# Kernel tuning notes

Hardware: AMD Instinct MI355X
Metric: run time of the kernel (lower is better)

The kernel has to match this reference:

```python
import jax, jax.numpy as jnp
import numpy as np

N = 8192      # nodes
E = 131072    # global edges
SDIM = 256    # scalar channels
VDIM = 64     # vector channels
EDIM = 128    # edge feature dim
L = 5         # num_layers
DIN = 2 * SDIM + EDIM + 4        # [s_src, s_tgt, e, d, a, |p_src|, |p_tgt|]
DOUT = SDIM + 2 * VDIM + 1 + EDIM  # [m_s, w_v1, w_v2, w_p, e_new]
HID = SDIM


def setup_inputs() -> dict:
    key = jax.random.key(0)
    ks = jax.random.split(key, 12)
    s = jax.random.normal(ks[0], (N, SDIM), jnp.float32)
    v = 0.1 * jax.random.normal(ks[1], (N, 3, VDIM), jnp.float32)
    p = 3.0 * jax.random.normal(ks[2], (N, 3), jnp.float32)
    e = jax.random.normal(ks[3], (E, EDIM), jnp.float32)
    edge_index = jax.random.randint(ks[4], (2, E), 0, N, dtype=jnp.int32)
    W1 = jax.random.normal(ks[5], (L, DIN, HID), jnp.float32) / np.sqrt(DIN)
    W2 = jax.random.normal(ks[6], (L, HID, DOUT), jnp.float32) / np.sqrt(HID)
    U1 = jax.random.normal(ks[7], (L, SDIM, SDIM), jnp.float32) / np.sqrt(SDIM)
    U2 = jax.random.normal(ks[8], (L, SDIM, SDIM), jnp.float32) / np.sqrt(SDIM)
    return {
        's': s, 'v': v, 'p': p, 'e': e, 'edge_index': edge_index,
        'ln_g': jnp.ones((L, SDIM), jnp.float32),
        'ln_b': jnp.zeros((L, SDIM), jnp.float32),
        'W1': W1, 'b1': jnp.zeros((L, HID), jnp.float32),
        'W2': W2, 'b2': jnp.zeros((L, DOUT), jnp.float32),
        'U1': U1, 'bU1': jnp.zeros((L, SDIM), jnp.float32),
        'U2': U2, 'bU2': jnp.zeros((L, SDIM), jnp.float32),
    }


def _edge_attrs(edge_index, pos):
    # Faithful to calculate_edge_attrs (sqrt=True, no ligand-pocket branch)
    src, tgt = edge_index[0], edge_index[1]
    r = pos[tgt] - pos[src]                                   # [E,3]
    a = jnp.sum(pos[tgt] * pos[src], axis=-1)                 # [E]
    d = jnp.sqrt(jnp.clip(jnp.sum(r * r, axis=-1), 1e-6, None))
    r_norm = r / (1.0 + d[:, None])
    return d, a, r_norm


def reference(s, v, p, e, edge_index, ln_g, ln_b, W1, b1, W2, b2, U1, bU1, U2, bU2):
    src, tgt = edge_index[0], edge_index[1]
    d, a, rn = _edge_attrs(edge_index, p)
    # in-degree counts for 'mean' vector/position aggregation
    cnt = jnp.clip(jax.ops.segment_sum(jnp.ones((E,), s.dtype), tgt, num_segments=N), 1.0)
    for i in range(L):
        # LayerNorm on scalar channels (vectors passed through)
        mu = jnp.mean(s, axis=-1, keepdims=True)
        var = jnp.mean((s - mu) ** 2, axis=-1, keepdims=True)
        s_ln = ln_g[i] * (s - mu) * jax.lax.rsqrt(var + 1e-5) + ln_b[i]
        pn = jnp.linalg.norm(p, axis=-1, keepdims=True)       # use_pos_norm features
        # gather-compute edge messages
        feat = jnp.concatenate(
            [s_ln[src], s_ln[tgt], e, d[:, None], a[:, None], pn[src], pn[tgt]], axis=-1)
        h = jax.nn.silu(feat @ W1[i] + b1[i])                 # [E,HID]
        out = h @ W2[i] + b2[i]                               # [E,DOUT]
        m_s = out[:, :SDIM]
        wv1 = out[:, SDIM:SDIM + VDIM]
        wv2 = out[:, SDIM + VDIM:SDIM + 2 * VDIM]
        wp = out[:, SDIM + 2 * VDIM:SDIM + 2 * VDIM + 1]
        e_new = out[:, SDIM + 2 * VDIM + 1:]
        has_v = 0.0 if i == 0 else 1.0                        # has_v_in = (i > 0)
        m_v = has_v * wv1[:, None, :] * v[src] + wv2[:, None, :] * rn[:, :, None]  # [E,3,VDIM]
        m_p = jnp.tanh(wp) * rn                               # [E,3]
        # scatter-aggregate (sum for scalars, mean for vectors/positions)
        s = s + jax.ops.segment_sum(m_s, tgt, num_segments=N)
        v = v + jax.ops.segment_sum(m_v, tgt, num_segments=N) / cnt[:, None, None]
        p = p + jax.ops.segment_sum(m_p, tgt, num_segments=N) / cnt[:, None]
        if i < L - 1:                                         # use_mlp_update = (i < num_layers - 1)
            s = s + jax.nn.silu(s @ U1[i] + bU1[i]) @ U2[i] + bU2[i]
        e = jax.nn.silu(e_new)
        # recompute_edge_attributes=True: redo gather/distance math on new positions
        d, a, rn = _edge_attrs(edge_index, p)
    return s, v, e, p
```

## Files before the change

### kernel.cpp

```cpp
#include <hip/hip_runtime.h>
#include <hip/hip_bf16.h>

namespace {

constexpr int NN   = 8192;
constexpr int NE   = 131072;
constexpr int SD   = 256;
constexpr int ED   = 128;
constexpr int NL   = 5;
constexpr int DINc = 644;
constexpr int KE   = 160;
constexpr int TE   = 5;
constexpr int T2   = 8;
constexpr int DOUTc= 513;
constexpr int HIDc = 256;

typedef __bf16 bf16x8 __attribute__((ext_vector_type(8)));
typedef float  f32x4  __attribute__((ext_vector_type(4)));

__device__ __forceinline__ float siluf(float x) { return x / (1.0f + __expf(-x)); }

__device__ __forceinline__ void gl_lds16(const void* gsrc, void* lds_uniform_base) {
  __builtin_amdgcn_global_load_lds(
      (const __attribute__((address_space(1))) unsigned int*)gsrc,
      (__attribute__((address_space(3))) unsigned int*)lds_uniform_base, 16, 0, 0);
}

__device__ __forceinline__ void wait_vm4() {
  asm volatile("s_waitcnt vmcnt(4)" ::: "memory");
  __builtin_amdgcn_sched_barrier(0);
}
__device__ __forceinline__ void wait_vm0() {
  asm volatile("s_waitcnt vmcnt(0)" ::: "memory");
  __builtin_amdgcn_sched_barrier(0);
}

__device__ __host__ __forceinline__ int swz(int kc) { return (kc * 5) & 7; }
__device__ __forceinline__ int apos(int kc, int row) { return kc * 64  + (row ^ swz(kc)); }
__device__ __forceinline__ int bpos(int kc, int n)   { return kc * 256 + (n   ^ swz(kc)); }

enum { SRC_BF16 = 1 };

struct GemmArgs {
  const __hip_bfloat16* Wt;
  const float* bias;
  const __hip_bfloat16* Abf;
  __hip_bfloat16* bf_out;
  const __hip_bfloat16* Wtb;
  const float* biasb;
  __hip_bfloat16* bf_outb;
  int dual;
};

__device__ __forceinline__ uint4 cvt8f(const float* p) {
  alignas(16) __hip_bfloat16 t8[8];
#pragma unroll
  for (int i = 0; i < 8; i++) t8[i] = __float2bfloat16(p[i]);
  return *(const uint4*)t8;
}

template<int KTOT, int BM>
__global__ __launch_bounds__(256) void gemm_k(GemmArgs g) {
  constexpr int T = KTOT / 32;
  constexpr int NC = KTOT / 8;
  constexpr int RPT = 256 / BM;
  constexpr int RMASK = RPT - 1;
  __shared__ alignas(16) unsigned short Apan[NC * BM * 8];
  __shared__ alignas(16) unsigned short Bsh[2][4 * 256 * 8];
  const int tid = threadIdx.x, lane = tid & 63, wave = tid >> 6;
  const int l16 = lane & 15, lhi = lane >> 4;
  const __hip_bfloat16* wtp = g.Wt;
  const float* biasp = g.bias;
  __hip_bfloat16* outp = g.bf_out;
  int blk = blockIdx.x;
  {
    const int half = gridDim.x >> 1;
    if (g.dual && blk >= half) { blk -= half; wtp = g.Wtb; biasp = g.biasb; outp = g.bf_outb; }
  }
  const int row0 = blk * BM;
  const int ar = tid / RPT, aq = tid % RPT;
  const int arow = row0 + ar;
  f32x4 acc[BM / 16][4] = {};

  auto issueB = [&](int t, int buf) {
    const __hip_bfloat16* src = wtp + (size_t)t * 1024 * 8;
    unsigned short* dst = &Bsh[buf][0];
#pragma unroll
    for (int i = 0; i < 4; i++)
      gl_lds16(src + (size_t)(i * 256 + wave * 64 + lane) * 8, dst + (i * 256 + wave * 64) * 8);
  };

  issueB(0, 0);
#pragma unroll
  for (int j = 0; j < NC / RPT; j++) {
    const int c = j * RPT + aq;
    uint4 o = *(const uint4*)(g.Abf + (size_t)arow * KTOT + c * 8);
    *(uint4*)&Apan[(c * BM + (ar ^ swz(aq))) * 8] = o;
  }
  __syncthreads();

  int cur = 0;
  for (int t = 0; t < T; ++t) {
    if (t + 1 < T) { issueB(t + 1, cur ^ 1); wait_vm4(); }
    else           { wait_vm0(); }
    bf16x8 bfr[4];
#pragma unroll
    for (int f = 0; f < 4; f++)
      bfr[f] = *(const bf16x8*)&Bsh[cur][bpos(lhi, wave * 64 + f * 16 + l16) * 8];
#pragma unroll
    for (int fr = 0; fr < BM / 16; fr++) {
      const int kc = t * 4 + lhi;
      const bf16x8 afr = *(const bf16x8*)&Apan[(kc * BM + ((fr * 16 + l16) ^ swz(kc & RMASK))) * 8];
#pragma unroll
      for (int fc = 0; fc < 4; fc++)
        acc[fr][fc] = __builtin_amdgcn_mfma_f32_16x16x32_bf16(afr, bfr[fc], acc[fr][fc], 0, 0, 0);
    }
    cur ^= 1;
  }

#pragma unroll
  for (int fr = 0; fr < BM / 16; fr++) {
#pragma unroll
    for (int fc = 0; fc < 4; fc++) {
      const int n = wave * 64 + fc * 16 + l16;
#pragma unroll
      for (int r = 0; r < 4; r++) {
        const int row = row0 + fr * 16 + lhi * 4 + r;
        outp[(size_t)row * HIDc + n] = __float2bfloat16(acc[fr][fc][r] + biasp[n]);
      }
    }
  }
}

struct Node3Args {
  const __hip_bfloat16* W2a;
  const __hip_bfloat16* U1s;
  const __hip_bfloat16* U2s;
  const __hip_bfloat16* W1an;
  const __hip_bfloat16* W1bn;
  const float* b2L;
  const float* bU1;
  const float* bU2;
  const float* b1n;
  const float* lng;
  const float* lnb;
  const float* Hagg;
  const int* rawcnt;
  float* s_out;
  __hip_bfloat16* p1;
  __hip_bfloat16* p2;
};

template<int LAST>
__global__ __launch_bounds__(256) void node3_k(Node3Args g) {
  constexpr int BM = 32, RPT = 8, NC = 32, T = 8;
  __shared__ alignas(16) unsigned short Apan[NC * BM * 8];
  __shared__ alignas(16) unsigned short Bsh[2][4 * 256 * 8];
  __shared__ float red[2][4][32];
  const int tid = threadIdx.x, lane = tid & 63, wave = tid >> 6;
  const int l16 = lane & 15, lhi = lane >> 4;
  const int row0 = blockIdx.x * BM;
  const int ar = tid >> 3, aq = tid & 7;

  auto issueB = [&](const __hip_bfloat16* W, int t, int buf) {
    const __hip_bfloat16* src = W + (size_t)t * 1024 * 8;
    unsigned short* dst = &Bsh[buf][0];
#pragma unroll
    for (int i = 0; i < 4; i++)
      gl_lds16(src + (size_t)(i * 256 + wave * 64 + lane) * 8, dst + (i * 256 + wave * 64) * 8);
  };

  f32x4 acc[4][2];
  auto kloop = [&](const __hip_bfloat16* W) {
#pragma unroll
    for (int i = 0; i < 4; i++)
#pragma unroll
      for (int j = 0; j < 2; j++) acc[i][j] = f32x4{0.f, 0.f, 0.f, 0.f};
    int cur = 0;
    for (int t = 0; t < T; ++t) {
      if (t + 1 < T) { issueB(W, t + 1, cur ^ 1); wait_vm4(); }
      else           { wait_vm0(); }
      bf16x8 wfr[4], afr[2];
#pragma unroll
      for (int f = 0; f < 4; f++)
        wfr[f] = *(const bf16x8*)&Bsh[cur][bpos(lhi, wave * 64 + f * 16 + l16) * 8];
#pragma unroll
      for (int f = 0; f < 2; f++) {
        const int kc = t * 4 + lhi;
        afr[f] = *(const bf16x8*)&Apan[(kc * BM + ((f * 16 + l16) ^ swz(kc & 7))) * 8];
      }
#pragma unroll
      for (int fr = 0; fr < 4; fr++)
#pragma unroll
        for (int fc = 0; fc < 2; fc++)
          acc[fr][fc] = __builtin_amdgcn_mfma_f32_16x16x32_bf16(wfr[fr], afr[fc], acc[fr][fc], 0, 0, 0);
      cur ^= 1;
    }
  };

  issueB(g.W2a, 0, 0);
#pragma unroll
  for (int j = 0; j < NC / RPT; j++) {
    const int c = j * RPT + aq;
    uint4 o = cvt8f(g.Hagg + (size_t)(row0 + ar) * SD + c * 8);
    *(uint4*)&Apan[(c * BM + (ar ^ swz(aq))) * 8] = o;
  }
  __syncthreads();

  kloop(g.W2a);
  __syncthreads();
  if constexpr (!LAST) issueB(g.U1s, 0, 0);

#pragma unroll
  for (int fr = 0; fr < 4; fr++) {
    const int nb = wave * 64 + fr * 16 + lhi * 4;
    const int kc = nb >> 3, off = nb & 7;
    const f32x4 b4 = *(const f32x4*)(g.b2L + nb);
#pragma unroll
    for (int fc = 0; fc < 2; fc++) {
      const int row = fc * 16 + l16;
      const float rc = (float)g.rawcnt[row0 + row];
      float* sp = g.s_out + (size_t)(row0 + row) * SD + nb;
      f32x4 sold = *(const f32x4*)sp;
      alignas(8) __hip_bfloat16 hb[4];
      f32x4 s1;
#pragma unroll
      for (int r = 0; r < 4; r++) {
        s1[r] = sold[r] + acc[fr][fc][r] + rc * b4[r];
        hb[r] = __float2bfloat16(s1[r]);
      }
      *(f32x4*)sp = s1;
      if constexpr (!LAST)
        *(uint2*)&Apan[(kc * BM + (row ^ swz(kc & 7))) * 8 + off] = *(const uint2*)hb;
    }
  }
  if constexpr (LAST) return;

  __syncthreads();

  kloop(g.U1s);
  __syncthreads();
  issueB(g.U2s, 0, 0);
#pragma unroll
  for (int fr = 0; fr < 4; fr++) {
    const int nb = wave * 64 + fr * 16 + lhi * 4;
    const int kc = nb >> 3, off = nb & 7;
    const f32x4 b4 = *(const f32x4*)(g.bU1 + nb);
#pragma unroll
    for (int fc = 0; fc < 2; fc++) {
      const int row = fc * 16 + l16;
      alignas(8) __hip_bfloat16 hb[4];
#pragma unroll
      for (int r = 0; r < 4; r++)
        hb[r] = __float2bfloat16(siluf(acc[fr][fc][r] + b4[r]));
      *(uint2*)&Apan[(kc * BM + (row ^ swz(kc & 7))) * 8 + off] = *(const uint2*)hb;
    }
  }
  __syncthreads();

  kloop(g.U2s);
  float psum[2] = {0.f, 0.f}, psq[2] = {0.f, 0.f};
#pragma unroll
  for (int fr = 0; fr < 4; fr++) {
    const int nb = wave * 64 + fr * 16 + lhi * 4;
    const f32x4 b4 = *(const f32x4*)(g.bU2 + nb);
#pragma unroll
    for (int fc = 0; fc < 2; fc++) {
      const int row = fc * 16 + l16;
      float* sp = g.s_out + (size_t)(row0 + row) * SD + nb;
      f32x4 sv = *(const f32x4*)sp;
#pragma unroll
      for (int r = 0; r < 4; r++) {
        sv[r] += acc[fr][fc][r] + b4[r];
        psum[fc] += sv[r];
        psq[fc] += sv[r] * sv[r];
      }
      *(f32x4*)sp = sv;
      acc[fr][fc] = sv;
    }
  }
#pragma unroll
  for (int fc = 0; fc < 2; fc++) {
    psum[fc] += __shfl_xor(psum[fc], 16); psum[fc] += __shfl_xor(psum[fc], 32);
    psq[fc]  += __shfl_xor(psq[fc], 16);  psq[fc]  += __shfl_xor(psq[fc], 32);
  }
  if (lane < 16) {
    red[0][wave][lane] = psum[0]; red[0][wave][16 + lane] = psum[1];
    red[1][wave][lane] = psq[0];  red[1][wave][16 + lane] = psq[1];
  }
  __syncthreads();

  float mu2[2], rs2[2];
#pragma unroll
  for (int fc = 0; fc < 2; fc++) {
    const int ri = fc * 16 + l16;
    const float S = red[0][0][ri] + red[0][1][ri] + red[0][2][ri] + red[0][3][ri];
    const float Q = red[1][0][ri] + red[1][1][ri] + red[1][2][ri] + red[1][3][ri];
    const float mu = S * (1.0f / SD);
    const float var = Q * (1.0f / SD) - mu * mu;
    mu2[fc] = mu; rs2[fc] = rsqrtf(var + 1e-5f);
  }
#pragma unroll
  for (int fr = 0; fr < 4; fr++) {
    const int nb = wave * 64 + fr * 16 + lhi * 4;
    const int kc = nb >> 3, off = nb & 7;
    const f32x4 g4 = *(const f32x4*)(g.lng + nb);
    const f32x4 bb4 = *(const f32x4*)(g.lnb + nb);
#pragma unroll
    for (int fc = 0; fc < 2; fc++) {
      const int row = fc * 16 + l16;
      alignas(8) __hip_bfloat16 hb[4];
#pragma unroll
      for (int r = 0; r < 4; r++)
        hb[r] = __float2bfloat16(g4[r] * (acc[fr][fc][r] - mu2[fc]) * rs2[fc] + bb4[r]);
      *(uint2*)&Apan[(kc * BM + (row ^ swz(kc & 7))) * 8 + off] = *(const uint2*)hb;
    }
  }
  issueB(g.W1an, 0, 0);
  __syncthreads();

  kloop(g.W1an);
#pragma unroll
  for (int fr = 0; fr < 4; fr++) {
    const int nb = wave * 64 + fr * 16 + lhi * 4;
    const f32x4 b4 = *(const f32x4*)(g.b1n + nb);
#pragma unroll
    for (int fc = 0; fc < 2; fc++) {
      const int row = fc * 16 + l16;
      alignas(8) __hip_bfloat16 hb[4];
#pragma unroll
      for (int r = 0; r < 4; r++)
        hb[r] = __float2bfloat16(acc[fr][fc][r] + b4[r]);
      *(uint2*)(g.p1 + (size_t)(row0 + row) * SD + nb) = *(const uint2*)hb;
    }
  }
  issueB(g.W1bn, 0, 0);
  kloop(g.W1bn);
#pragma unroll
  for (int fr = 0; fr < 4; fr++) {
    const int nb = wave * 64 + fr * 16 + lhi * 4;
#pragma unroll
    for (int fc = 0; fc < 2; fc++) {
      const int row = fc * 16 + l16;
      alignas(8) __hip_bfloat16 hb[4];
#pragma unroll
      for (int r = 0; r < 4; r++)
        hb[r] = __float2bfloat16(acc[fr][fc][r]);
      *(uint2*)(g.p2 + (size_t)(row0 + row) * SD + nb) = *(const uint2*)hb;
    }
  }
}

struct FusedArgs {
  const __hip_bfloat16* W1e;
  const __hip_bfloat16* W2s;
  const float* b2L;
  const int* src; const int* tgt;
  const int* rank;
  const float* pos;
  const __hip_bfloat16* e_bf;
  const __hip_bfloat16* p1;
  const __hip_bfloat16* p2;
  const __hip_bfloat16* w384;
  float* rnp;
  float* mp;
  __hip_bfloat16* h_out;
  __hip_bfloat16* wv_out;
  __hip_bfloat16* e_bf_out;
  float* e_f32_out;
  int write_e_f32;
};

__global__ __launch_bounds__(256) void fused_k(FusedArgs g) {
  __shared__ alignas(16) unsigned short Ash[4 * 64 * 8];
  __shared__ alignas(16) unsigned short Bsh[2][4 * 256 * 8];
  __shared__ alignas(16) unsigned short Hsh[32 * 64 * 8];
  __shared__ float wps[4][64];
  __shared__ float RnL[64][3];
  __shared__ unsigned int EdL[64][2];
  __shared__ int Rk[64];
  const int tid = threadIdx.x, lane = tid & 63, wave = tid >> 6;
  const int l16 = lane & 15, lhi = lane >> 4;
  const int row0 = blockIdx.x * 64;
  const int ar = tid >> 2, aq = tid & 3;
  const int arow = row0 + ar;
  const int sn = g.src[arow], tn = g.tgt[arow];

  auto issueW = [&](const __hip_bfloat16* W, int t, int buf) {
    const __hip_bfloat16* src = W + (size_t)t * 1024 * 8;
    unsigned short* dst = &Bsh[buf][0];
#pragma unroll
    for (int i = 0; i < 4; i++)
      gl_lds16(src + (size_t)(i * 256 + wave * 64 + lane) * 8, dst + (i * 256 + wave * 64) * 8);
  };
  auto loadA = [&](int t, uint4& o) {
    if (t < 4) {
      o = *(const uint4*)(g.e_bf + (size_t)arow * ED + t * 32 + aq * 8);
    } else {
      o.x = o.y = o.z = o.w = 0;
      if (aq == 0) { o.x = EdL[ar][0]; o.y = EdL[ar][1]; }
    }
  };

  uint4 a;
  loadA(0, a);
  issueW(g.W1e, 0, 0);

  if (tid < 64) {
    const int e = row0 + tid;
    const int rk = g.rank[e];
    Rk[tid] = rk;
    const int s_ = g.src[e], t_ = g.tgt[e];
    const float sx = g.pos[s_ * 3], sy = g.pos[s_ * 3 + 1], sz = g.pos[s_ * 3 + 2];
    const float tx = g.pos[t_ * 3], ty = g.pos[t_ * 3 + 1], tz = g.pos[t_ * 3 + 2];
    const float rx = tx - sx, ry = ty - sy, rz = tz - sz;
    const float av = tx * sx + ty * sy + tz * sz;
    const float rr = rx * rx + ry * ry + rz * rz;
    const float d = sqrtf(fmaxf(rr, 1e-6f));
    const float inv = 1.0f / (1.0f + d);
    const float r0 = rx * inv, r1 = ry * inv, r2 = rz * inv;
    RnL[tid][0] = r0; RnL[tid][1] = r1; RnL[tid][2] = r2;
    g.rnp[rk * 3] = r0; g.rnp[rk * 3 + 1] = r1; g.rnp[rk * 3 + 2] = r2;
    alignas(8) __hip_bfloat16 q[4];
    q[0] = __float2bfloat16(d);
    q[1] = __float2bfloat16(av);
    q[2] = __float2bfloat16(sqrtf(sx * sx + sy * sy + sz * sz));
    q[3] = __float2bfloat16(sqrtf(tx * tx + ty * ty + tz * tz));
    EdL[tid][0] = ((const unsigned*)q)[0];
    EdL[tid][1] = ((const unsigned*)q)[1];
  }

#pragma unroll
  for (int j = 0; j < 8; j++) {
    const int c = j * 4 + aq;
    uint4 r1 = *(const uint4*)(g.p1 + (size_t)sn * SD + c * 8);
    uint4 r2 = *(const uint4*)(g.p2 + (size_t)tn * SD + c * 8);
    const __hip_bfloat16* h1 = (const __hip_bfloat16*)&r1;
    const __hip_bfloat16* h2 = (const __hip_bfloat16*)&r2;
    alignas(16) __hip_bfloat16 o8[8];
#pragma unroll
    for (int m = 0; m < 8; m++)
      o8[m] = __float2bfloat16(__bfloat162float(h1[m]) + __bfloat162float(h2[m]));
    *(uint4*)&Hsh[(c * 64 + (ar ^ swz(aq))) * 8] = *(const uint4*)o8;
  }

  f32x4 acc1[4][4] = {};
  int cur = 0;
  for (int t = 0; t < TE; ++t) {
    *(uint4*)&Ash[apos(aq, ar) * 8] = a;
    __syncthreads();
    if (t + 1 < TE) { issueW(g.W1e, t + 1, cur ^ 1); loadA(t + 1, a); }
    bf16x8 wfr[4], efr[4];
#pragma unroll
    for (int f = 0; f < 4; f++) {
      wfr[f] = *(const bf16x8*)&Bsh[cur][bpos(lhi, wave * 64 + f * 16 + l16) * 8];
      efr[f] = *(const bf16x8*)&Ash[apos(lhi, f * 16 + l16) * 8];
    }
#pragma unroll
    for (int fr = 0; fr < 4; fr++)
#pragma unroll
      for (int fc = 0; fc < 4; fc++)
        acc1[fr][fc] = __builtin_amdgcn_mfma_f32_16x16x32_bf16(wfr[fr], efr[fc], acc1[fr][fc], 0, 0, 0);
    __syncthreads();
    cur ^= 1;
  }

  issueW(g.W2s, 0, 0);

  float pw[4] = {0.f, 0.f, 0.f, 0.f};
#pragma unroll
  for (int fr = 0; fr < 4; fr++) {
    const int nb = wave * 64 + fr * 16 + lhi * 4;
    const int kc = nb >> 3, off = nb & 7;
    uint2 wr = *(const uint2*)(g.w384 + nb);
    const __hip_bfloat16* w4 = (const __hip_bfloat16*)&wr;
#pragma unroll
    for (int fc = 0; fc < 4; fc++) {
      const int row = fc * 16 + l16;
      unsigned short* slot = &Hsh[(kc * 64 + (row ^ swz(kc & 3))) * 8 + off];
      uint2 pr = *(const uint2*)slot;
      const __hip_bfloat16* pp = (const __hip_bfloat16*)&pr;
      alignas(8) __hip_bfloat16 hb[4];
#pragma unroll
      for (int r = 0; r < 4; r++) {
        const float hv = siluf(acc1[fr][fc][r] + __bfloat162float(pp[r]));
        hb[r] = __float2bfloat16(hv);
        pw[fc] += hv * __bfloat162float(w4[r]);
      }
      *(uint2*)slot = *(const uint2*)hb;
      *(uint2*)(g.h_out + (size_t)Rk[row] * HIDc + nb) = *(const uint2*)hb;
    }
  }

#pragma unroll
  for (int fc = 0; fc < 4; fc++) {
    pw[fc] += __shfl_xor(pw[fc], 16);
    pw[fc] += __shfl_xor(pw[fc], 32);
  }
  if (lane < 16) {
#pragma unroll
    for (int fc = 0; fc < 4; fc++) wps[wave][fc * 16 + lane] = pw[fc];
  }
  __syncthreads();
  if (tid < 64) {
    const float s = wps[0][tid] + wps[1][tid] + wps[2][tid] + wps[3][tid];
    const float wpt = tanhf(s + g.b2L[384]);
    const int rk = Rk[tid];
#pragma unroll
    for (int c = 0; c < 3; c++)
      g.mp[(size_t)rk * 3 + c] = wpt * RnL[tid][c];
  }

  f32x4 acc2[4][4] = {};
  cur = 0;
  for (int t = 0; t < T2; ++t) {
    if (t + 1 < T2) { issueW(g.W2s, t + 1, cur ^ 1); wait_vm4(); }
    else            { wait_vm0(); }
    bf16x8 afr[4], bfr[4];
#pragma unroll
    for (int f = 0; f < 4; f++) {
      const int kc = t * 4 + lhi;
      afr[f] = *(const bf16x8*)&Hsh[(kc * 64 + ((f * 16 + l16) ^ swz(lhi))) * 8];
      bfr[f] = *(const bf16x8*)&Bsh[cur][bpos(lhi, wave * 64 + f * 16 + l16) * 8];
    }
#pragma unroll
    for (int fr = 0; fr < 4; fr++)
#pragma unroll
      for (int fc = 0; fc < 4; fc++)
        acc2[fr][fc] = __builtin_amdgcn_mfma_f32_16x16x32_bf16(afr[fr], bfr[fc], acc2[fr][fc], 0, 0, 0);
    cur ^= 1;
  }

#pragma unroll
  for (int fr = 0; fr < 4; fr++) {
#pragma unroll
    for (int fc = 0; fc < 4; fc++) {
      const int n = wave * 64 + fc * 16 + l16;
#pragma unroll
      for (int r = 0; r < 4; r++) {
        const int lr = fr * 16 + lhi * 4 + r;
        const int row = row0 + lr;
        const float valf = acc2[fr][fc][r];
        if (n < 128) {
          g.wv_out[(size_t)Rk[lr] * 128 + n] = __float2bfloat16(valf + g.b2L[256 + n]);
        } else {
          const float sv = siluf(valf + g.b2L[257 + n]);
          g.e_bf_out[(size_t)row * ED + (n - 128)] = __float2bfloat16(sv);
          if (g.write_e_f32) g.e_f32_out[(size_t)row * ED + (n - 128)] = sv;
        }
      }
    }
  }
}

__global__ __launch_bounds__(256) void ln_k(const float* __restrict__ s,
                                            const float* __restrict__ gl, const float* __restrict__ bl,
                                            __hip_bfloat16* __restrict__ s_ln) {
  const int wave = threadIdx.x >> 6, lane = threadIdx.x & 63;
  const int node = blockIdx.x * 4 + wave;
  const float* srow = s + (size_t)node * SD;
  float x[4], sum = 0.f, sq = 0.f;
#pragma unroll
  for (int i = 0; i < 4; i++) { x[i] = srow[lane * 4 + i]; sum += x[i]; sq += x[i] * x[i]; }
#pragma unroll
  for (int off = 1; off < 64; off <<= 1) { sum += __shfl_xor(sum, off); sq += __shfl_xor(sq, off); }
  const float mu = sum * (1.0f / SD);
  const float var = sq * (1.0f / SD) - mu * mu;
  const float rstd = rsqrtf(var + 1e-5f);
#pragma unroll
  for (int i = 0; i < 4; i++) {
    const int c = lane * 4 + i;
    s_ln[(size_t)node * SD + c] = __float2bfloat16(gl[c] * (x[i] - mu) * rstd + bl[c]);
  }
}

__global__ void cvt_e_k(const float* __restrict__ e, __hip_bfloat16* __restrict__ ebf) {
  const int i = blockIdx.x * blockDim.x + threadIdx.x;
  const float* p = e + (size_t)i * 8;
  alignas(16) __hip_bfloat16 t8[8];
#pragma unroll
  for (int j = 0; j < 8; j++) t8[j] = __float2bfloat16(p[j]);
  *(uint4*)(ebf + (size_t)i * 8) = *(const uint4*)t8;
}

__global__ void count_k(const int* __restrict__ tgt, int* __restrict__ rawcnt) {
  const int e = blockIdx.x * blockDim.x + threadIdx.x;
  if (e < NE) atomicAdd(&rawcnt[tgt[e]], 1);
}

__global__ __launch_bounds__(256) void scan_k(const int* __restrict__ rawcnt, int* __restrict__ off) {
  __shared__ int ts[256];
  const int tid = threadIdx.x;
  const int base = tid * 32;
  int local[32];
  int s = 0;
#pragma unroll
  for (int i = 0; i < 32; i++) { local[i] = s; s += rawcnt[base + i]; }
  ts[tid] = s;
  __syncthreads();
  if (tid == 0) {
    int acc = 0;
    for (int i = 0; i < 256; i++) { int t = ts[i]; ts[i] = acc; acc += t; }
    off[NN] = acc;
  }
  __syncthreads();
  const int pre = ts[tid];
#pragma unroll
  for (int i = 0; i < 32; i++) off[base + i] = pre + local[i];
}

__global__ void scatter_k(const int* __restrict__ tgt, const int* __restrict__ srcp,
                          const int* __restrict__ off,
                          int* __restrict__ cursor, int* __restrict__ rank, int* __restrict__ psrc) {
  const int e = blockIdx.x * blockDim.x + threadIdx.x;
  if (e < NE) {
    const int t = tgt[e];
    const int pos = off[t] + atomicAdd(&cursor[t], 1);
    rank[e] = pos;
    psrc[pos] = srcp[e];
  }
}

__global__ __launch_bounds__(256) void agg_k(const int* __restrict__ off, const int* __restrict__ psrc,
                                             const __hip_bfloat16* __restrict__ h,
                                             const __hip_bfloat16* __restrict__ wv,
                                             const float* __restrict__ mp,
                                             const float* __restrict__ rnp,
                                             const float* __restrict__ v_old,
                                             float* __restrict__ v_new,
                                             float* __restrict__ Hagg,
                                             float* __restrict__ p_o,
                                             int hasv) {
  const int n = blockIdx.x;
  const int c = threadIdx.x;
  const int e0 = off[n], e1 = off[n + 1];
  const int c3 = c >> 6, ln = c & 63;
  float hs = 0.f, vs = 0.f, ps = 0.f;
  int j = e0;
  for (; j + 2 <= e1; j += 2) {
    const float h0 = __bfloat162float(h[(size_t)j * HIDc + c]);
    const float h1 = __bfloat162float(h[(size_t)(j + 1) * HIDc + c]);
    hs += h0 + h1;
    if (c < 192) {
      const int s0 = psrc[j], s1 = psrc[j + 1];
      float m0 = __bfloat162float(wv[(size_t)j * 128 + 64 + ln]) * rnp[j * 3 + c3];
      float m1 = __bfloat162float(wv[(size_t)(j + 1) * 128 + 64 + ln]) * rnp[(j + 1) * 3 + c3];
      if (hasv) {
        m0 += __bfloat162float(wv[(size_t)j * 128 + ln]) * v_old[(size_t)s0 * 192 + c];
        m1 += __bfloat162float(wv[(size_t)(j + 1) * 128 + ln]) * v_old[(size_t)s1 * 192 + c];
      }
      vs += m0 + m1;
    } else if (c < 195) {
      ps += mp[j * 3 + (c - 192)] + mp[(j + 1) * 3 + (c - 192)];
    }
  }
  for (; j < e1; j++) {
    hs += __bfloat162float(h[(size_t)j * HIDc + c]);
    if (c < 192) {
      float mv = __bfloat162float(wv[(size_t)j * 128 + 64 + ln]) * rnp[j * 3 + c3];
      if (hasv) mv += __bfloat162float(wv[(size_t)j * 128 + ln]) * v_old[(size_t)psrc[j] * 192 + c];
      vs += mv;
    } else if (c < 195) {
      ps += mp[j * 3 + (c - 192)];
    }
  }
  Hagg[(size_t)n * HIDc + c] = hs;
  const float inv = 1.0f / fmaxf((float)(e1 - e0), 1.0f);
  if (c < 192)      v_new[(size_t)n * 192 + c] = v_old[(size_t)n * 192 + c] + vs * inv;
  else if (c < 195) p_o[n * 3 + (c - 192)]    += ps * inv;
}

__global__ void zero_k(float* __restrict__ ptr, int n) {
  const int i = blockIdx.x * blockDim.x + threadIdx.x;
  if (i < n) ptr[i] = 0.f;
}

__global__ void prep_w1abs_k(const float* __restrict__ W1, __hip_bfloat16* __restrict__ W1aS,
                             __hip_bfloat16* __restrict__ W1bS) {
  const int idx = blockIdx.x * blockDim.x + threadIdx.x;
  if (idx >= NL * T2 * 1024) return;
  const int p = idx & 1023, t = (idx >> 10) % T2, l = idx / (T2 * 1024);
  const int kc = p >> 8, n = (p & 255) ^ swz(kc);
  alignas(16) __hip_bfloat16 a8[8], b8[8];
#pragma unroll
  for (int j = 0; j < 8; j++) {
    const int k = t * 32 + kc * 8 + j;
    a8[j] = __float2bfloat16(W1[((size_t)l * DINc + k) * HIDc + n]);
    b8[j] = __float2bfloat16(W1[((size_t)l * DINc + 256 + k) * HIDc + n]);
  }
  *(uint4*)(W1aS + (size_t)idx * 8) = *(const uint4*)a8;
  *(uint4*)(W1bS + (size_t)idx * 8) = *(const uint4*)b8;
}

__global__ void prep_w1es_k(const float* __restrict__ W1, __hip_bfloat16* __restrict__ W1eS) {
  const int idx = blockIdx.x * blockDim.x + threadIdx.x;
  if (idx >= NL * TE * 1024) return;
  const int p = idx & 1023, t = (idx >> 10) % TE, l = idx / (TE * 1024);
  const int kc = p >> 8, n = (p & 255) ^ swz(kc);
  alignas(16) __hip_bfloat16 e8[8];
#pragma unroll
  for (int j = 0; j < 8; j++) {
    const int k = t * 32 + kc * 8 + j;
    const int row = (k < 128) ? (512 + k) : ((k < 132) ? (640 + (k - 128)) : -1);
    e8[j] = __float2bfloat16(row >= 0 ? W1[((size_t)l * DINc + row) * HIDc + n] : 0.f);
  }
  *(uint4*)(W1eS + (size_t)idx * 8) = *(const uint4*)e8;
}

__global__ void prep_w2s_k(const float* __restrict__ W2, __hip_bfloat16* __restrict__ W2sS,
                           __hip_bfloat16* __restrict__ W2aS) {
  const int idx = blockIdx.x * blockDim.x + threadIdx.x;
  if (idx >= NL * T2 * 1024) return;
  const int p = idx & 1023, t = (idx >> 10) & 7, l = idx >> 13;
  const int kc = p >> 8, n = (p & 255) ^ swz(kc);
  const float* W2l = W2 + (size_t)l * HIDc * DOUTc;
  const int cs = (n < 128) ? (256 + n) : (257 + n);
  alignas(16) __hip_bfloat16 s8[8], a8[8];
#pragma unroll
  for (int j = 0; j < 8; j++) {
    const int k = t * 32 + kc * 8 + j;
    s8[j] = __float2bfloat16(W2l[(size_t)k * DOUTc + cs]);
    a8[j] = __float2bfloat16(W2l[(size_t)k * DOUTc + n]);
  }
  *(uint4*)(W2sS + (size_t)idx * 8) = *(const uint4*)s8;
  *(uint4*)(W2aS + (size_t)idx * 8) = *(const uint4*)a8;
}

__global__ void prep_uts_k(const float* __restrict__ U1, const float* __restrict__ U2,
                           __hip_bfloat16* __restrict__ U1S, __hip_bfloat16* __restrict__ U2S) {
  const int idx = blockIdx.x * blockDim.x + threadIdx.x;
  if (idx >= NL * T2 * 1024) return;
  const int p = idx & 1023, t = (idx >> 10) & 7, l = idx >> 13;
  const int kc = p >> 8, n = (p & 255) ^ swz(kc);
  alignas(16) __hip_bfloat16 u1[8], u2[8];
#pragma unroll
  for (int j = 0; j < 8; j++) {
    const int k = t * 32 + kc * 8 + j;
    u1[j] = __float2bfloat16(U1[((size_t)l * HIDc + k) * HIDc + n]);
    u2[j] = __float2bfloat16(U2[((size_t)l * HIDc + k) * HIDc + n]);
  }
  *(uint4*)(U1S + (size_t)idx * 8) = *(const uint4*)u1;
  *(uint4*)(U2S + (size_t)idx * 8) = *(const uint4*)u2;
}

__global__ void prep_w384_k(const float* __restrict__ W2, __hip_bfloat16* __restrict__ w384) {
  const int idx = blockIdx.x * blockDim.x + threadIdx.x;
  if (idx >= NL * HIDc) return;
  const int k = idx & 255, l = idx >> 8;
  w384[idx] = __float2bfloat16(W2[((size_t)l * HIDc + k) * DOUTc + 384]);
}

}

extern "C" void kernel_launch(void* const* d_in, const int* in_sizes, int n_in,
                              void* d_out, int out_size, void* d_ws, size_t ws_size,
                              hipStream_t stream) {
  (void)in_sizes; (void)n_in; (void)out_size; (void)ws_size;
  const float* s_in = (const float*)d_in[0];
  const float* v_in = (const float*)d_in[1];
  const float* p_in = (const float*)d_in[2];
  const float* e_in = (const float*)d_in[3];
  const int*   ei   = (const int*)d_in[4];
  const float* ln_g = (const float*)d_in[5];
  const float* ln_b = (const float*)d_in[6];
  const float* W1   = (const float*)d_in[7];
  const float* b1   = (const float*)d_in[8];
  const float* W2   = (const float*)d_in[9];
  const float* b2   = (const float*)d_in[10];
  const float* U1   = (const float*)d_in[11];
  const float* bU1  = (const float*)d_in[12];
  const float* U2   = (const float*)d_in[13];
  const float* bU2  = (const float*)d_in[14];

  float* s_o = (float*)d_out;
  float* v_o = s_o + (size_t)NN * SD;
  float* e_o = v_o + (size_t)NN * 192;
  float* p_o = e_o + (size_t)NE * ED;

  const int* srcp = ei;
  const int* tgtp = ei + NE;

  char* wp = (char*)d_ws;
  auto alloc = [&](size_t bytes) -> char* {
    char* r = wp; wp += (bytes + 255) & ~(size_t)255; return r;
  };
  __hip_bfloat16* s_ln = (__hip_bfloat16*)alloc((size_t)NN * SD * 2);
  __hip_bfloat16* hbuf = (__hip_bfloat16*)alloc((size_t)NE * HIDc * 2);
  __hip_bfloat16* ebf  = (__hip_bfloat16*)alloc((size_t)NE * ED * 2);
  __hip_bfloat16* wvbuf= (__hip_bfloat16*)alloc((size_t)NE * 128 * 2);
  __hip_bfloat16* p1buf= (__hip_bfloat16*)alloc((size_t)NN * SD * 2);
  __hip_bfloat16* p2buf= (__hip_bfloat16*)alloc((size_t)NN * SD * 2);
  float* rnpbuf= (float*)alloc((size_t)NE * 3 * 4);
  float* Hagg  = (float*)alloc((size_t)NN * SD * 4);
  float* vprev = (float*)alloc((size_t)NN * 192 * 4);
  float* mpbuf = (float*)alloc((size_t)NE * 3 * 4);
  float* zerobias = (float*)alloc(256 * 4);
  int*   rawcnt= (int*)alloc((size_t)NN * 4);
  int*   offb  = (int*)alloc((size_t)(NN + 1) * 4);
  int*   cursor= (int*)alloc((size_t)NN * 4);
  int*   rankb = (int*)alloc((size_t)NE * 4);
  int*   psrcb = (int*)alloc((size_t)NE * 4);
  __hip_bfloat16* W1aS = (__hip_bfloat16*)alloc((size_t)NL * T2 * 1024 * 8 * 2);
  __hip_bfloat16* W1bS = (__hip_bfloat16*)alloc((size_t)NL * T2 * 1024 * 8 * 2);
  __hip_bfloat16* W1eS = (__hip_bfloat16*)alloc((size_t)NL * TE * 1024 * 8 * 2);
  __hip_bfloat16* W2sS = (__hip_bfloat16*)alloc((size_t)NL * T2 * 1024 * 8 * 2);
  __hip_bfloat16* W2aS = (__hip_bfloat16*)alloc((size_t)NL * T2 * 1024 * 8 * 2);
  __hip_bfloat16* U1S  = (__hip_bfloat16*)alloc((size_t)NL * T2 * 1024 * 8 * 2);
  __hip_bfloat16* U2S  = (__hip_bfloat16*)alloc((size_t)NL * T2 * 1024 * 8 * 2);
  __hip_bfloat16* w384 = (__hip_bfloat16*)alloc((size_t)NL * HIDc * 2);

  hipMemcpyAsync(s_o, s_in, (size_t)NN * SD * 4, hipMemcpyDeviceToDevice, stream);
  hipMemcpyAsync(vprev, v_in, (size_t)NN * 192 * 4, hipMemcpyDeviceToDevice, stream);
  hipMemcpyAsync(p_o, p_in, (size_t)NN * 3 * 4, hipMemcpyDeviceToDevice, stream);

  prep_w1abs_k<<<(NL * T2 * 1024 + 255) / 256, 256, 0, stream>>>(W1, W1aS, W1bS);
  prep_w1es_k<<<(NL * TE * 1024 + 255) / 256, 256, 0, stream>>>(W1, W1eS);
  prep_w2s_k<<<(NL * T2 * 1024 + 255) / 256, 256, 0, stream>>>(W2, W2sS, W2aS);
  prep_uts_k<<<(NL * T2 * 1024 + 255) / 256, 256, 0, stream>>>(U1, U2, U1S, U2S);
  prep_w384_k<<<(NL * HIDc + 255) / 256, 256, 0, stream>>>(W2, w384);
  cvt_e_k<<<NE * ED / 8 / 256, 256, 0, stream>>>(e_in, ebf);
  zero_k<<<1, 256, 0, stream>>>(zerobias, 256);

  zero_k<<<(NN + 255) / 256, 256, 0, stream>>>((float*)rawcnt, NN);
  zero_k<<<(NN + 255) / 256, 256, 0, stream>>>((float*)cursor, NN);
  count_k<<<NE / 256, 256, 0, stream>>>(tgtp, rawcnt);
  scan_k<<<1, 256, 0, stream>>>(rawcnt, offb);
  scatter_k<<<NE / 256, 256, 0, stream>>>(tgtp, srcp, offb, cursor, rankb, psrcb);

  ln_k<<<NN / 4, 256, 0, stream>>>(s_o, ln_g, ln_b, s_ln);
  GemmArgs gp{};
  gp.Wt = W1aS; gp.bias = b1; gp.bf_out = p1buf;
  gp.Wtb = W1bS; gp.biasb = zerobias; gp.bf_outb = p2buf;
  gp.Abf = s_ln; gp.dual = 1;
  gemm_k<256, 64><<<2 * NN / 64, 256, 0, stream>>>(gp);

  for (int l = 0; l < NL; l++) {
    FusedArgs gf{};
    gf.W1e = W1eS + (size_t)l * TE * 1024 * 8;
    gf.W2s = W2sS + (size_t)l * T2 * 1024 * 8;
    gf.b2L = b2 + l * DOUTc;
    gf.src = srcp; gf.tgt = tgtp; gf.rank = rankb;
    gf.pos = p_o; gf.e_bf = ebf;
    gf.p1 = p1buf; gf.p2 = p2buf; gf.w384 = w384 + l * HIDc;
    gf.rnp = rnpbuf; gf.mp = mpbuf;
    gf.h_out = hbuf; gf.wv_out = wvbuf; gf.e_bf_out = ebf; gf.e_f32_out = e_o;
    gf.write_e_f32 = (l == NL - 1) ? 1 : 0;
    fused_k<<<NE / 64, 256, 0, stream>>>(gf);

    const float* vold = (l & 1) ? (const float*)v_o : (const float*)vprev;
    float* vnew = (l & 1) ? vprev : v_o;
    agg_k<<<NN, 256, 0, stream>>>(offb, psrcb, hbuf, wvbuf, mpbuf, rnpbuf,
                                  vold, vnew, Hagg, p_o, (l > 0) ? 1 : 0);

    Node3Args gn{};
    gn.W2a = W2aS + (size_t)l * T2 * 1024 * 8;
    gn.U1s = U1S + (size_t)l * T2 * 1024 * 8;
    gn.U2s = U2S + (size_t)l * T2 * 1024 * 8;
    gn.b2L = b2 + l * DOUTc; gn.bU1 = bU1 + l * HIDc; gn.bU2 = bU2 + l * HIDc;
    gn.Hagg = Hagg; gn.rawcnt = rawcnt; gn.s_out = s_o;
    if (l < NL - 1) {
      gn.W1an = W1aS + (size_t)(l + 1) * T2 * 1024 * 8;
      gn.W1bn = W1bS + (size_t)(l + 1) * T2 * 1024 * 8;
      gn.b1n = b1 + (l + 1) * HIDc;
      gn.lng = ln_g + (l + 1) * SD; gn.lnb = ln_b + (l + 1) * SD;
      gn.p1 = p1buf; gn.p2 = p2buf;
      node3_k<0><<<NN / 32, 256, 0, stream>>>(gn);
    } else {
      node3_k<1><<<NN / 32, 256, 0, stream>>>(gn);
    }
  }
}
```

Baseline: 1.020 ms.

## Stage whole edge-feature tile in LDS and drop per-step barriers in first GEMM

Loads all edge features and edge attributes into the shared H buffer before the first GEMM. The first GEMM loop then runs without two block barriers per k-step, using vmcnt waits on the async weight loads, like the second GEMM. The gathered node projections are prefetched early into registers and written to LDS after the first GEMM. This removes the separate A buffer and per-step synchronisation, but raises register pressure. Without a barrier, the double-buffered weight tiles may be overwritten while other waves still read them.

```diff
diff --git a/kernel.cpp b/kernel.cpp
--- a/kernel.cpp
+++ b/kernel.cpp
@@ -36,8 +36,8 @@
 }
 
 __device__ __host__ __forceinline__ int swz(int kc) { return (kc * 5) & 7; }
-__device__ __forceinline__ int apos(int kc, int row) { return kc * 64  + (row ^ swz(kc)); }
 __device__ __forceinline__ int bpos(int kc, int n)   { return kc * 256 + (n   ^ swz(kc)); }
+__device__ __forceinline__ int ppos(int kc, int row) { return kc * 64 + (row ^ swz(kc & 3)); }
 
 enum { SRC_BF16 = 1 };
 
@@ -372,12 +372,10 @@
 };
 
 __global__ __launch_bounds__(256) void fused_k(FusedArgs g) {
-  __shared__ alignas(16) unsigned short Ash[4 * 64 * 8];
   __shared__ alignas(16) unsigned short Bsh[2][4 * 256 * 8];
   __shared__ alignas(16) unsigned short Hsh[32 * 64 * 8];
   __shared__ float wps[4][64];
   __shared__ float RnL[64][3];
-  __shared__ unsigned int EdL[64][2];
   __shared__ int Rk[64];
   const int tid = threadIdx.x, lane = tid & 63, wave = tid >> 6;
   const int l16 = lane & 15, lhi = lane >> 4;
@@ -393,18 +391,16 @@
     for (int i = 0; i < 4; i++)
       gl_lds16(src + (size_t)(i * 256 + wave * 64 + lane) * 8, dst + (i * 256 + wave * 64) * 8);
   };
-  auto loadA = [&](int t, uint4& o) {
-    if (t < 4) {
-      o = *(const uint4*)(g.e_bf + (size_t)arow * ED + t * 32 + aq * 8);
-    } else {
-      o.x = o.y = o.z = o.w = 0;
-      if (aq == 0) { o.x = EdL[ar][0]; o.y = EdL[ar][1]; }
-    }
-  };
-
-  uint4 a;
-  loadA(0, a);
+
   issueW(g.W1e, 0, 0);
+
+  uint4 r1[8], r2[8];
+#pragma unroll
+  for (int j = 0; j < 8; j++) {
+    const int c = j * 4 + aq;
+    r1[j] = *(const uint4*)(g.p1 + (size_t)sn * SD + c * 8);
+    r2[j] = *(const uint4*)(g.p2 + (size_t)tn * SD + c * 8);
+  }
 
   if (tid < 64) {
     const int e = row0 + tid;
@@ -418,54 +414,69 @@
     const float rr = rx * rx + ry * ry + rz * rz;
     const float d = sqrtf(fmaxf(rr, 1e-6f));
     const float inv = 1.0f / (1.0f + d);
-    const float r0 = rx * inv, r1 = ry * inv, r2 = rz * inv;
-    RnL[tid][0] = r0; RnL[tid][1] = r1; RnL[tid][2] = r2;
-    g.rnp[rk * 3] = r0; g.rnp[rk * 3 + 1] = r1; g.rnp[rk * 3 + 2] = r2;
-    alignas(8) __hip_bfloat16 q[4];
-    q[0] = __float2bfloat16(d);
-    q[1] = __float2bfloat16(av);
-    q[2] = __float2bfloat16(sqrtf(sx * sx + sy * sy + sz * sz));
-    q[3] = __float2bfloat16(sqrtf(tx * tx + ty * ty + tz * tz));
-    EdL[tid][0] = ((const unsigned*)q)[0];
-    EdL[tid][1] = ((const unsigned*)q)[1];
-  }
-
+    const float r0 = rx * inv, r1v = ry * inv, r2v = rz * inv;
+    RnL[tid][0] = r0; RnL[tid][1] = r1v; RnL[tid][2] = r2v;
+    g.rnp[rk * 3] = r0; g.rnp[rk * 3 + 1] = r1v; g.rnp[rk * 3 + 2] = r2v;
+    alignas(16) __hip_bfloat16 q8[8];
+    q8[0] = __float2bfloat16(d);
+    q8[1] = __float2bfloat16(av);
+    q8[2] = __float2bfloat16(sqrtf(sx * sx + sy * sy + sz * sz));
+    q8[3] = __float2bfloat16(sqrtf(tx * tx + ty * ty + tz * tz));
+    q8[4] = q8[5] = q8[6] = q8[7] = __float2bfloat16(0.0f);
+    *(uint4*)&Hsh[ppos(16, tid) * 8] = *(const uint4*)q8;
+  } else {
+  }
+  if (aq > 0) {
+    uint4 z; z.x = z.y = z.z = z.w = 0;
+    *(uint4*)&Hsh[ppos(16 + aq, ar) * 8] = z;
+  }
+#pragma unroll
+  for (int j = 0; j < 4; j++) {
+    const int c = j * 4 + aq;
+    uint4 o = *(const uint4*)(g.e_bf + (size_t)arow * ED + c * 8);
+    *(uint4*)&Hsh[ppos(c, ar) * 8] = o;
+  }
+  __syncthreads();
+
+  uint4 ps[8];
 #pragma unroll
   for (int j = 0; j < 8; j++) {
-    const int c = j * 4 + aq;
-    uint4 r1 = *(const uint4*)(g.p1 + (size_t)sn * SD + c * 8);
-    uint4 r2 = *(const uint4*)(g.p2 + (size_t)tn * SD + c * 8);
-    const __hip_bfloat16* h1 = (const __hip_bfloat16*)&r1;
-    const __hip_bfloat16* h2 = (const __hip_bfloat16*)&r2;
+    const __hip_bfloat16* h1 = (const __hip_bfloat16*)&r1[j];
+    const __hip_bfloat16* h2 = (const __hip_bfloat16*)&r2[j];
     alignas(16) __hip_bfloat16 o8[8];
 #pragma unroll
     for (int m = 0; m < 8; m++)
       o8[m] = __float2bfloat16(__bfloat162float(h1[m]) + __bfloat162float(h2[m]));
-    *(uint4*)&Hsh[(c * 64 + (ar ^ swz(aq))) * 8] = *(const uint4*)o8;
+    ps[j] = *(const uint4*)o8;
   }
 
   f32x4 acc1[4][4] = {};
   int cur = 0;
   for (int t = 0; t < TE; ++t) {
-    *(uint4*)&Ash[apos(aq, ar) * 8] = a;
-    __syncthreads();
-    if (t + 1 < TE) { issueW(g.W1e, t + 1, cur ^ 1); loadA(t + 1, a); }
+    if (t + 1 < TE) { issueW(g.W1e, t + 1, cur ^ 1); wait_vm4(); }
+    else            { wait_vm0(); }
     bf16x8 wfr[4], efr[4];
 #pragma unroll
     for (int f = 0; f < 4; f++) {
       wfr[f] = *(const bf16x8*)&Bsh[cur][bpos(lhi, wave * 64 + f * 16 + l16) * 8];
-      efr[f] = *(const bf16x8*)&Ash[apos(lhi, f * 16 + l16) * 8];
+      efr[f] = *(const bf16x8*)&Hsh[ppos(t * 4 + lhi, f * 16 + l16) * 8];
     }
 #pragma unroll
     for (int fr = 0; fr < 4; fr++)
 #pragma unroll
       for (int fc = 0; fc < 4; fc++)
         acc1[fr][fc] = __builtin_amdgcn_mfma_f32_16x16x32_bf16(wfr[fr], efr[fc], acc1[fr][fc], 0, 0, 0);
-    __syncthreads();
     cur ^= 1;
   }
+  __syncthreads();
 
   issueW(g.W2s, 0, 0);
+#pragma unroll
+  for (int j = 0; j < 8; j++) {
+    const int c = j * 4 + aq;
+    *(uint4*)&Hsh[ppos(c, ar) * 8] = ps[j];
+  }
+  __syncthreads();
 
   float pw[4] = {0.f, 0.f, 0.f, 0.f};
 #pragma unroll
@@ -477,7 +488,7 @@
 #pragma unroll
     for (int fc = 0; fc < 4; fc++) {
       const int row = fc * 16 + l16;
-      unsigned short* slot = &Hsh[(kc * 64 + (row ^ swz(kc & 3))) * 8 + off];
+      unsigned short* slot = &Hsh[ppos(kc, row) * 8 + off];
       uint2 pr = *(const uint2*)slot;
       const __hip_bfloat16* pp = (const __hip_bfloat16*)&pr;
       alignas(8) __hip_bfloat16 hb[4];
@@ -519,8 +530,7 @@
     bf16x8 afr[4], bfr[4];
 #pragma unroll
     for (int f = 0; f < 4; f++) {
-      const int kc = t * 4 + lhi;
-      afr[f] = *(const bf16x8*)&Hsh[(kc * 64 + ((f * 16 + l16) ^ swz(lhi))) * 8];
+      afr[f] = *(const bf16x8*)&Hsh[ppos(t * 4 + lhi, f * 16 + l16) * 8];
       bfr[f] = *(const bf16x8*)&Bsh[cur][bpos(lhi, wave * 64 + f * 16 + l16) * 8];
     }
 #pragma unroll
```

Measured after the change: 1.404 ms. 37.7% more time.

## Process edges in target-sorted order to make fused kernel writes contiguous

Applied to the files above, without the earlier changes.

Edge features are permuted into target-sorted (CSR) order once at setup, and the fused edge kernel then iterates over edges in that sorted order. Its h, wv, mp and rn outputs are now written contiguously by row instead of scattered through a rank indirection. Only the final-layer fp32 edge output is scattered back through the inverse permutation. Gathers of p2 by target become highly local, since consecutive edges share targets. In exchange, cvt_e performs a gathered read and the scatter kernel writes two extra index arrays.

```diff
diff --git a/kernel.cpp b/kernel.cpp
--- a/kernel.cpp
+++ b/kernel.cpp
@@ -355,8 +355,9 @@
   const __hip_bfloat16* W1e;
   const __hip_bfloat16* W2s;
   const float* b2L;
-  const int* src; const int* tgt;
-  const int* rank;
+  const int* psrc;
+  const int* ptgt;
+  const int* iperm;
   const float* pos;
   const __hip_bfloat16* e_bf;
   const __hip_bfloat16* p1;
@@ -378,13 +379,13 @@
   __shared__ float wps[4][64];
   __shared__ float RnL[64][3];
   __shared__ unsigned int EdL[64][2];
-  __shared__ int Rk[64];
+  __shared__ int Ei[64];
   const int tid = threadIdx.x, lane = tid & 63, wave = tid >> 6;
   const int l16 = lane & 15, lhi = lane >> 4;
   const int row0 = blockIdx.x * 64;
   const int ar = tid >> 2, aq = tid & 3;
   const int arow = row0 + ar;
-  const int sn = g.src[arow], tn = g.tgt[arow];
+  const int sn = g.psrc[arow], tn = g.ptgt[arow];
 
   auto issueW = [&](const __hip_bfloat16* W, int t, int buf) {
     const __hip_bfloat16* src = W + (size_t)t * 1024 * 8;
@@ -408,9 +409,8 @@
 
   if (tid < 64) {
     const int e = row0 + tid;
-    const int rk = g.rank[e];
-    Rk[tid] = rk;
-    const int s_ = g.src[e], t_ = g.tgt[e];
+    Ei[tid] = g.iperm[e];
+    const int s_ = g.psrc[e], t_ = g.ptgt[e];
     const float sx = g.pos[s_ * 3], sy = g.pos[s_ * 3 + 1], sz = g.pos[s_ * 3 + 2];
     const float tx = g.pos[t_ * 3], ty = g.pos[t_ * 3 + 1], tz = g.pos[t_ * 3 + 2];
     const float rx = tx - sx, ry = ty - sy, rz = tz - sz;
@@ -420,7 +420,7 @@
     const float inv = 1.0f / (1.0f + d);
     const float r0 = rx * inv, r1 = ry * inv, r2 = rz * inv;
     RnL[tid][0] = r0; RnL[tid][1] = r1; RnL[tid][2] = r2;
-    g.rnp[rk * 3] = r0; g.rnp[rk * 3 + 1] = r1; g.rnp[rk * 3 + 2] = r2;
+    g.rnp[e * 3] = r0; g.rnp[e * 3 + 1] = r1; g.rnp[e * 3 + 2] = r2;
     alignas(8) __hip_bfloat16 q[4];
     q[0] = __float2bfloat16(d);
     q[1] = __float2bfloat16(av);
@@ -488,7 +488,7 @@
         pw[fc] += hv * __bfloat162float(w4[r]);
       }
       *(uint2*)slot = *(const uint2*)hb;
-      *(uint2*)(g.h_out + (size_t)Rk[row] * HIDc + nb) = *(const uint2*)hb;
+      *(uint2*)(g.h_out + (size_t)(row0 + row) * HIDc + nb) = *(const uint2*)hb;
     }
   }
 
@@ -505,10 +505,10 @@
   if (tid < 64) {
     const float s = wps[0][tid] + wps[1][tid] + wps[2][tid] + wps[3][tid];
     const float wpt = tanhf(s + g.b2L[384]);
-    const int rk = Rk[tid];
+    const int e = row0 + tid;
 #pragma unroll
     for (int c = 0; c < 3; c++)
-      g.mp[(size_t)rk * 3 + c] = wpt * RnL[tid][c];
+      g.mp[(size_t)e * 3 + c] = wpt * RnL[tid][c];
   }
 
   f32x4 acc2[4][4] = {};
@@ -542,11 +542,11 @@
         const int row = row0 + lr;
         const float valf = acc2[fr][fc][r];
         if (n < 128) {
-          g.wv_out[(size_t)Rk[lr] * 128 + n] = __float2bfloat16(valf + g.b2L[256 + n]);
+          g.wv_out[(size_t)row * 128 + n] = __float2bfloat16(valf + g.b2L[256 + n]);
         } else {
           const float sv = siluf(valf + g.b2L[257 + n]);
           g.e_bf_out[(size_t)row * ED + (n - 128)] = __float2bfloat16(sv);
-          if (g.write_e_f32) g.e_f32_out[(size_t)row * ED + (n - 128)] = sv;
+          if (g.write_e_f32) g.e_f32_out[(size_t)Ei[lr] * ED + (n - 128)] = sv;
         }
       }
     }
@@ -574,13 +574,16 @@
   }
 }
 
-__global__ void cvt_e_k(const float* __restrict__ e, __hip_bfloat16* __restrict__ ebf) {
-  const int i = blockIdx.x * blockDim.x + threadIdx.x;
-  const float* p = e + (size_t)i * 8;
+__global__ void cvt_e_k(const float* __restrict__ e, const int* __restrict__ iperm,
+                        __hip_bfloat16* __restrict__ ebf) {
+  const int idx = blockIdx.x * blockDim.x + threadIdx.x;
+  const int pos = idx >> 4, c = idx & 15;
+  const int src_e = iperm[pos];
+  const float* p = e + (size_t)src_e * ED + c * 8;
   alignas(16) __hip_bfloat16 t8[8];
 #pragma unroll
   for (int j = 0; j < 8; j++) t8[j] = __float2bfloat16(p[j]);
-  *(uint4*)(ebf + (size_t)i * 8) = *(const uint4*)t8;
+  *(uint4*)(ebf + (size_t)pos * ED + c * 8) = *(const uint4*)t8;
 }
 
 __global__ void count_k(const int* __restrict__ tgt, int* __restrict__ rawcnt) {
@@ -610,14 +613,15 @@
 }
 
 __global__ void scatter_k(const int* __restrict__ tgt, const int* __restrict__ srcp,
-                          const int* __restrict__ off,
-                          int* __restrict__ cursor, int* __restrict__ rank, int* __restrict__ psrc) {
+                          const int* __restrict__ off, int* __restrict__ cursor,
+                          int* __restrict__ psrc, int* __restrict__ ptgt, int* __restrict__ iperm) {
   const int e = blockIdx.x * blockDim.x + threadIdx.x;
   if (e < NE) {
     const int t = tgt[e];
     const int pos = off[t] + atomicAdd(&cursor[t], 1);
-    rank[e] = pos;
     psrc[pos] = srcp[e];
+    ptgt[pos] = t;
+    iperm[pos] = e;
   }
 }
 
@@ -798,8 +802,9 @@
   int*   rawcnt= (int*)alloc((size_t)NN * 4);
   int*   offb  = (int*)alloc((size_t)(NN + 1) * 4);
   int*   cursor= (int*)alloc((size_t)NN * 4);
-  int*   rankb = (int*)alloc((size_t)NE * 4);
   int*   psrcb = (int*)alloc((size_t)NE * 4);
+  int*   ptgtb = (int*)alloc((size_t)NE * 4);
+  int*   ipermb= (int*)alloc((size_t)NE * 4);
   __hip_bfloat16* W1aS = (__hip_bfloat16*)alloc((size_t)NL * T2 * 1024 * 8 * 2);
   __hip_bfloat16* W1bS = (__hip_bfloat16*)alloc((size_t)NL * T2 * 1024 * 8 * 2);
   __hip_bfloat16* W1eS = (__hip_bfloat16*)alloc((size_t)NL * TE * 1024 * 8 * 2);
@@ -818,14 +823,14 @@
   prep_w2s_k<<<(NL * T2 * 1024 + 255) / 256, 256, 0, stream>>>(W2, W2sS, W2aS);
   prep_uts_k<<<(NL * T2 * 1024 + 255) / 256, 256, 0, stream>>>(U1, U2, U1S, U2S);
   prep_w384_k<<<(NL * HIDc + 255) / 256, 256, 0, stream>>>(W2, w384);
-  cvt_e_k<<<NE * ED / 8 / 256, 256, 0, stream>>>(e_in, ebf);
   zero_k<<<1, 256, 0, stream>>>(zerobias, 256);
 
   zero_k<<<(NN + 255) / 256, 256, 0, stream>>>((float*)rawcnt, NN);
   zero_k<<<(NN + 255) / 256, 256, 0, stream>>>((float*)cursor, NN);
   count_k<<<NE / 256, 256, 0, stream>>>(tgtp, rawcnt);
   scan_k<<<1, 256, 0, stream>>>(rawcnt, offb);
-  scatter_k<<<NE / 256, 256, 0, stream>>>(tgtp, srcp, offb, cursor, rankb, psrcb);
+  scatter_k<<<NE / 256, 256, 0, stream>>>(tgtp, srcp, offb, cursor, psrcb, ptgtb, ipermb);
+  cvt_e_k<<<NE * 16 / 256, 256, 0, stream>>>(e_in, ipermb, ebf);
 
   ln_k<<<NN / 4, 256, 0, stream>>>(s_o, ln_g, ln_b, s_ln);
   GemmArgs gp{};
@@ -839,7 +844,7 @@
     gf.W1e = W1eS + (size_t)l * TE * 1024 * 8;
     gf.W2s = W2sS + (size_t)l * T2 * 1024 * 8;
     gf.b2L = b2 + l * DOUTc;
-    gf.src = srcp; gf.tgt = tgtp; gf.rank = rankb;
+    gf.psrc = psrcb; gf.ptgt = ptgtb; gf.iperm = ipermb;
     gf.pos = p_o; gf.e_bf = ebf;
     gf.p1 = p1buf; gf.p2 = p2buf; gf.w384 = w384 + l * HIDc;
     gf.rnp = rnpbuf; gf.mp = mpbuf;
```

After: 1.001 ms. About the same (-1.8%).
